# Kernel tuning notes

Measured on AMD Instinct MI355X. Metric: run time of the kernel, lower is better.

Reference implementation:

```python
import jax, jax.numpy as jnp
import numpy as np

# Domain bounds and training nu-range (from init_kwargs)
X_MIN, X_MAX = -1.0, 1.0
Y_MIN, Y_MAX = -1.0, 1.0
T_MIN, T_MAX = 0.0, 1.0
NU_MIN, NU_MAX = 0.01, 0.1

LAYERS = [4, 256, 256, 256, 256, 2]
N = 16384  # collocation points


def setup_inputs() -> dict:
    key = jax.random.key(0)
    ks = jax.random.split(key, 4 + 2 * (len(LAYERS) - 1))
    inp = {
        'x': jax.random.uniform(ks[0], (N, 1), minval=X_MIN, maxval=X_MAX, dtype=jnp.float32),
        'y': jax.random.uniform(ks[1], (N, 1), minval=Y_MIN, maxval=Y_MAX, dtype=jnp.float32),
        't': jax.random.uniform(ks[2], (N, 1), minval=T_MIN, maxval=T_MAX, dtype=jnp.float32),
        'nu': jax.random.uniform(ks[3], (N, 1), minval=NU_MIN, maxval=NU_MAX, dtype=jnp.float32),
    }
    # glorot_normal weights, zero biases (keras Dense defaults)
    for i in range(len(LAYERS) - 1):
        fan_in, fan_out = LAYERS[i], LAYERS[i + 1]
        std = (2.0 / (fan_in + fan_out)) ** 0.5
        inp[f'W{i}'] = std * jax.random.normal(ks[4 + 2 * i], (fan_in, fan_out), dtype=jnp.float32)
        inp[f'b{i}'] = jnp.zeros((fan_out,), dtype=jnp.float32)
    return inp


def _net(pt, nu, params):
    """MLP forward for a single point. pt: (3,) = (x, y, t); nu: scalar. Returns (2,) = (u, v)."""
    x, y, t = pt[0], pt[1], pt[2]
    h = jnp.stack([
        2.0 * (x - X_MIN) / (X_MAX - X_MIN) - 1.0,
        2.0 * (y - Y_MIN) / (Y_MAX - Y_MIN) - 1.0,
        2.0 * (t - T_MIN) / (T_MAX - T_MIN) - 1.0,
        2.0 * (nu - NU_MIN) / (NU_MAX - NU_MIN) - 1.0,
    ])
    for W, b in params[:-1]:
        z = h @ W + b
        h = z * jax.nn.sigmoid(z)  # swish
    W, b = params[-1]
    return h @ W + b


def _residual_point(pt, nu, params):
    """Burgers PDE residual (f_u, f_v) at one collocation point via nested forward-mode AD."""
    f = lambda p: _net(p, nu, params)
    uv = f(pt)                          # (2,)
    J = jax.jacfwd(f)(pt)               # (2,3): d(u,v)/d(x,y,t)
    H = jax.jacfwd(jax.jacfwd(f))(pt)   # (2,3,3)
    u, v = uv[0], uv[1]
    u_x, u_y, u_t = J[0, 0], J[0, 1], J[0, 2]
    v_x, v_y, v_t = J[1, 0], J[1, 1], J[1, 2]
    u_xx, u_yy = H[0, 0, 0], H[0, 1, 1]
    v_xx, v_yy = H[1, 0, 0], H[1, 1, 1]
    f_u = u_t + u * u_x + v * u_y - nu * (u_xx + u_yy)
    f_v = v_t + u * v_x + v * v_y - nu * (v_xx + v_yy)
    return jnp.stack([f_u, f_v])


def reference(x, y, t, nu, W0, b0, W1, b1, W2, b2, W3, b3, W4, b4):
    params = [(W0, b0), (W1, b1), (W2, b2), (W3, b3), (W4, b4)]
    pts = jnp.concatenate([x, y, t], axis=1)  # (N, 3)
    res = jax.vmap(lambda p, n: _residual_point(p, n, params))(pts, nu[:, 0])
    return res  # (N, 2) = [f_u, f_v]
```

## Files before the change

### kernel.cpp

```cpp
#include <hip/hip_runtime.h>

typedef _Float16 f16;
typedef _Float16 v8hf __attribute__((ext_vector_type(8)));
typedef _Float16 v4hf __attribute__((ext_vector_type(4)));
typedef _Float16 v2hf __attribute__((ext_vector_type(2)));
typedef __fp16   v2pk __attribute__((ext_vector_type(2)));
typedef float    v4f  __attribute__((ext_vector_type(4)));

#define NPTS 16384
#define PTS  16
#define NLAYER_ELEMS 65536

__device__ __forceinline__ v2hf pkrtz(float a, float b) {
    v2pk r = __builtin_amdgcn_cvt_pkrtz(a, b);
    return __builtin_bit_cast(v2hf, r);
}

__device__ __forceinline__ int swz(int m, int j) {
    return m * 256 + ((((j >> 3) ^ (m & 7)) << 3) | (j & 7));
}

__global__ void pack_weights(const float* __restrict__ W1, const float* __restrict__ W2,
                             const float* __restrict__ W3, f16* __restrict__ bh,
                             f16* __restrict__ bl) {
    const int b  = blockIdx.x;
    const int kg = b & 3;
    const int q  = (b >> 2) & 3;
    const int ks = (b >> 4) & 7;
    const int L  = b >> 7;
    const float* W = (L == 0) ? W1 : (L == 1) ? W2 : W3;
    const int n   = q * 64 + (threadIdx.x & 63);
    const int kk0 = kg * 8 + (threadIdx.x >> 6) * 2;
    f16 h[2], l[2];
    #pragma unroll
    for (int i = 0; i < 2; ++i) {
        float w = W[(ks * 32 + kk0 + i) * 256 + n];
        f16 hh = (f16)w;
        h[i] = hh;
        l[i] = (f16)(w - (float)hh);
    }
    size_t off = (size_t)L * NLAYER_ELEMS + (size_t)(ks * 256 + n) * 32 + kk0;
    *(v2hf*)(bh + off) = *(v2hf*)h;
    *(v2hf*)(bl + off) = *(v2hf*)l;
}

__device__ __forceinline__ void store_split(const float* a, int m, int nb,
                                            f16* __restrict__ Ah, f16* __restrict__ Al) {
    v2hf h01 = pkrtz(a[0], a[1]);
    v2hf h23 = pkrtz(a[2], a[3]);
    v2hf l01 = pkrtz(a[0] - (float)h01[0], a[1] - (float)h01[1]);
    v2hf l23 = pkrtz(a[2] - (float)h23[0], a[3] - (float)h23[1]);
    v4hf hi = { h01[0], h01[1], h23[0], h23[1] };
    v4hf lo = { l01[0], l01[1], l23[0], l23[1] };
    int idx = swz(m, nb);
    *(v4hf*)&Ah[idx] = hi;
    *(v4hf*)&Al[idx] = lo;
}

__global__ __launch_bounds__(512, 2) void pinn_burgers_kernel(
    const float* __restrict__ gx, const float* __restrict__ gy,
    const float* __restrict__ gt, const float* __restrict__ gnu,
    const float* __restrict__ W0, const float* __restrict__ b0,
    const float* __restrict__ b1, const float* __restrict__ b2,
    const float* __restrict__ b3,
    const float* __restrict__ W4, const float* __restrict__ b4,
    const f16* __restrict__ bh, const f16* __restrict__ bl,
    float* __restrict__ out)
{
    extern __shared__ f16 smem[];
    f16* __restrict__ Ah = smem;
    f16* __restrict__ Al = smem + 96 * 256;
    float* red = (float*)(smem + 2 * 96 * 256);
    float* pin = red + PTS * 12;

    const int tid  = threadIdx.x;
    const int lane = tid & 63;
    const int wv   = tid >> 6;
    const int ln   = lane & 15;
    const int quad = lane >> 4;
    const int lnx  = ln & 7;
    const int p0   = blockIdx.x * PTS;

    if (tid < 4 * PTS) {
        int c = tid >> 4, p = tid & 15;
        const float* src = (c == 0) ? gx : (c == 1) ? gy : (c == 2) ? gt : gnu;
        pin[c * PTS + p] = src[p0 + p];
    }
    __syncthreads();

    {
        const int j0 = wv * 32 + ln * 2;
        const int ph = quad * 4;
        float w00[2], w01[2], w02[2], w03[2], bb[2];
        #pragma unroll
        for (int e = 0; e < 2; ++e) {
            int j = j0 + e;
            w00[e] = W0[j]; w01[e] = W0[256 + j]; w02[e] = W0[512 + j]; w03[e] = W0[768 + j];
            bb[e] = b0[j];
        }
        #pragma unroll
        for (int pp = 0; pp < 4; ++pp) {
            int p = ph + pp;
            float hx = pin[0 * PTS + p];
            float hy = pin[1 * PTS + p];
            float ht = 2.f * pin[2 * PTS + p] - 1.f;
            float hn = 2.f * (pin[3 * PTS + p] - 0.01f) * (1.f / 0.09f) - 1.f;
            float a[6][2];
            #pragma unroll
            for (int e = 0; e < 2; ++e) {
                float z  = hx * w00[e] + hy * w01[e] + ht * w02[e] + hn * w03[e] + bb[e];
                float zx = w00[e], zy = w01[e], zt = 2.f * w02[e];
                float s  = 1.f / (1.f + __expf(-z));
                float g1 = s + z * s * (1.f - s);
                float g2 = s * (1.f - s) * (2.f + z * (1.f - 2.f * s));
                a[0][e] = z * s;
                a[1][e] = g1 * zx; a[2][e] = g1 * zy; a[3][e] = g1 * zt;
                a[4][e] = g2 * zx * zx; a[5][e] = g2 * zy * zy;
            }
            #pragma unroll
            for (int c = 0; c < 6; ++c) {
                int idx = swz(c * PTS + p, j0);
                v2hf hh = pkrtz(a[c][0], a[c][1]);
                v2hf ll = pkrtz(a[c][0] - (float)hh[0], a[c][1] - (float)hh[1]);
                *(v2hf*)&Ah[idx] = hh;
                *(v2hf*)&Al[idx] = ll;
            }
        }
    }
    __syncthreads();

    const float* bias_ptr[3] = { b1, b2, b3 };
    for (int L = 0; L < 3; ++L) {
        const f16* __restrict__ bhL = bh + (size_t)L * NLAYER_ELEMS;
        const f16* __restrict__ blL = bl + (size_t)L * NLAYER_ELEMS;
        const float* __restrict__ bv = bias_ptr[L];

        v4f acc[2][6];
        #pragma unroll
        for (int t = 0; t < 2; ++t)
            #pragma unroll
            for (int mt = 0; mt < 6; ++mt)
                acc[t][mt] = (v4f){0.f, 0.f, 0.f, 0.f};

        #pragma unroll 2
        for (int ks = 0; ks < 8; ++ks) {
            const int cb = (((4 * ks + quad) ^ lnx) << 3);
            v8hf a_h[6], a_l[6];
            #pragma unroll
            for (int mt = 0; mt < 6; ++mt) {
                const int rb = (mt * 16 + ln) * 256 + cb;
                a_h[mt] = *(const v8hf*)&Ah[rb];
                a_l[mt] = *(const v8hf*)&Al[rb];
            }
            v8hf w_h[2], w_l[2];
            #pragma unroll
            for (int t = 0; t < 2; ++t) {
                int n = wv * 32 + t * 16 + ln;
                size_t o = (size_t)(ks * 256 + n) * 32 + quad * 8;
                w_h[t] = *(const v8hf*)(bhL + o);
                w_l[t] = *(const v8hf*)(blL + o);
            }
            #pragma unroll
            for (int t = 0; t < 2; ++t)
                #pragma unroll
                for (int mt = 0; mt < 6; ++mt) {
                    acc[t][mt] = __builtin_amdgcn_mfma_f32_16x16x32_f16(w_h[t], a_h[mt], acc[t][mt], 0, 0, 0);
                    acc[t][mt] = __builtin_amdgcn_mfma_f32_16x16x32_f16(w_h[t], a_l[mt], acc[t][mt], 0, 0, 0);
                    acc[t][mt] = __builtin_amdgcn_mfma_f32_16x16x32_f16(w_l[t], a_h[mt], acc[t][mt], 0, 0, 0);
                }
        }
        __syncthreads();

        #pragma unroll
        for (int t = 0; t < 2; ++t) {
            const int nb = wv * 32 + t * 16 + quad * 4;
            const float4 bq = *(const float4*)(bv + nb);
            const float bb[4] = { bq.x, bq.y, bq.z, bq.w };
            float av[6][4];
            #pragma unroll
            for (int r = 0; r < 4; ++r) {
                float z   = acc[t][0][r] + bb[r];
                float zx  = acc[t][1][r];
                float zy  = acc[t][2][r];
                float zt  = acc[t][3][r];
                float zxx = acc[t][4][r];
                float zyy = acc[t][5][r];
                float s  = 1.f / (1.f + __expf(-z));
                float g1 = s + z * s * (1.f - s);
                float g2 = s * (1.f - s) * (2.f + z * (1.f - 2.f * s));
                av[0][r] = z * s;
                av[1][r] = g1 * zx;
                av[2][r] = g1 * zy;
                av[3][r] = g1 * zt;
                av[4][r] = g2 * zx * zx + g1 * zxx;
                av[5][r] = g2 * zy * zy + g1 * zyy;
            }
            #pragma unroll
            for (int c = 0; c < 6; ++c)
                store_split(av[c], c * 16 + ln, nb, Ah, Al);
        }
        __syncthreads();
    }

    #pragma unroll
    for (int d = 0; d < 24; ++d) {
        int D  = wv * 24 + d;
        int p  = D / 12;
        int rm = D % 12;
        int c  = rm >> 1;
        int o  = rm & 1;
        int m  = c * 16 + p;
        int k0 = lane * 4;
        int idx = swz(m, k0);
        v4hf hh = *(v4hf*)&Ah[idx];
        v4hf ll = *(v4hf*)&Al[idx];
        float partial = 0.f;
        #pragma unroll
        for (int i = 0; i < 4; ++i)
            partial += ((float)hh[i] + (float)ll[i]) * W4[(k0 + i) * 2 + o];
        #pragma unroll
        for (int off = 32; off > 0; off >>= 1)
            partial += __shfl_down(partial, off);
        if (lane == 0)
            red[p * 12 + rm] = partial + ((c == 0) ? b4[o] : 0.f);
    }
    __syncthreads();

    if (tid < PTS) {
        int p = tid;
        float u   = red[p*12+0],  v   = red[p*12+1];
        float ux  = red[p*12+2],  vx  = red[p*12+3];
        float uy  = red[p*12+4],  vy  = red[p*12+5];
        float ut  = red[p*12+6],  vt  = red[p*12+7];
        float uxx = red[p*12+8],  vxx = red[p*12+9];
        float uyy = red[p*12+10], vyy = red[p*12+11];
        float nuv = pin[3 * PTS + p];
        float fu = ut + u * ux + v * uy - nuv * (uxx + uyy);
        float fv = vt + u * vx + v * vy - nuv * (vxx + vyy);
        out[(p0 + p) * 2 + 0] = fu;
        out[(p0 + p) * 2 + 1] = fv;
    }
}

extern "C" void kernel_launch(void* const* d_in, const int* in_sizes, int n_in,
                              void* d_out, int out_size, void* d_ws, size_t ws_size,
                              hipStream_t stream) {
    const float* x  = (const float*)d_in[0];
    const float* y  = (const float*)d_in[1];
    const float* t  = (const float*)d_in[2];
    const float* nu = (const float*)d_in[3];
    const float* W0 = (const float*)d_in[4];
    const float* b0 = (const float*)d_in[5];
    const float* W1 = (const float*)d_in[6];
    const float* b1 = (const float*)d_in[7];
    const float* W2 = (const float*)d_in[8];
    const float* b2 = (const float*)d_in[9];
    const float* W3 = (const float*)d_in[10];
    const float* b3 = (const float*)d_in[11];
    const float* W4 = (const float*)d_in[12];
    const float* b4 = (const float*)d_in[13];
    float* o = (float*)d_out;

    f16* bh = (f16*)d_ws;
    f16* bl = bh + 3 * (size_t)NLAYER_ELEMS;

    const size_t shmem = 2 * 96 * 256 * sizeof(f16) + (PTS * 12 + 4 * PTS) * sizeof(float);
    static bool attr_set = false;
    (void)hipFuncSetAttribute((const void*)pinn_burgers_kernel,
                              hipFuncAttributeMaxDynamicSharedMemorySize, (int)shmem);

    hipLaunchKernelGGL(pack_weights, dim3(384), dim3(256), 0, stream, W1, W2, W3, bh, bl);
    hipLaunchKernelGGL(pinn_burgers_kernel, dim3(NPTS / PTS), dim3(512), shmem, stream,
                       x, y, t, nu, W0, b0, b1, b2, b3, W4, b4, bh, bl, o);
}
```

Baseline: 224.3 us.

## Retile hidden-layer MFMA work as 2x4 wave grid with interleaved row layout

Reorganizes the eight waves into a 2 (points) by 4 (neurons) grid so each wave computes 64 output neurons over 48 rows instead of 32 neurons over 96 rows. Activation rows are reordered so each 16-row tile mixes channels of 8 points, and the epilogue uses lane shuffles to reunite value and derivative channels for the same point. The aim is fewer LDS activation reads per MFMA, in exchange for more global weight fragments per wave, extra shuffles and lane selects in the epilogue.

```diff
diff --git a/kernel.cpp b/kernel.cpp
--- a/kernel.cpp
+++ b/kernel.cpp
@@ -18,6 +18,10 @@
 
 __device__ __forceinline__ int swz(int m, int j) {
     return m * 256 + ((((j >> 3) ^ (m & 7)) << 3) | (j & 7));
+}
+
+__device__ __forceinline__ int rowmap(int c, int p) {
+    return (p >> 3) * 48 + c * 8 + (p & 7);
 }
 
 __global__ void pack_weights(const float* __restrict__ W1, const float* __restrict__ W2,
@@ -76,6 +80,8 @@
     const int tid  = threadIdx.x;
     const int lane = tid & 63;
     const int wv   = tid >> 6;
+    const int nw   = wv & 3;
+    const int mw   = wv >> 2;
     const int ln   = lane & 15;
     const int quad = lane >> 4;
     const int lnx  = ln & 7;
@@ -89,8 +95,8 @@
     __syncthreads();
 
     {
-        const int j0 = wv * 32 + ln * 2;
-        const int ph = quad * 4;
+        const int j0 = nw * 64 + (lane & 31) * 2;
+        const int ph = mw * 8 + (lane >> 5) * 4;
         float w00[2], w01[2], w02[2], w03[2], bb[2];
         #pragma unroll
         for (int e = 0; e < 2; ++e) {
@@ -119,7 +125,7 @@
             }
             #pragma unroll
             for (int c = 0; c < 6; ++c) {
-                int idx = swz(c * PTS + p, j0);
+                int idx = swz(rowmap(c, p), j0);
                 v2hf hh = pkrtz(a[c][0], a[c][1]);
                 v2hf ll = pkrtz(a[c][0] - (float)hh[0], a[c][1] - (float)hh[1]);
                 *(v2hf*)&Ah[idx] = hh;
@@ -129,41 +135,42 @@
     }
     __syncthreads();
 
+    const int rbase = mw * 48;
     const float* bias_ptr[3] = { b1, b2, b3 };
     for (int L = 0; L < 3; ++L) {
         const f16* __restrict__ bhL = bh + (size_t)L * NLAYER_ELEMS;
         const f16* __restrict__ blL = bl + (size_t)L * NLAYER_ELEMS;
         const float* __restrict__ bv = bias_ptr[L];
 
-        v4f acc[2][6];
-        #pragma unroll
-        for (int t = 0; t < 2; ++t)
-            #pragma unroll
-            for (int mt = 0; mt < 6; ++mt)
+        v4f acc[4][3];
+        #pragma unroll
+        for (int t = 0; t < 4; ++t)
+            #pragma unroll
+            for (int mt = 0; mt < 3; ++mt)
                 acc[t][mt] = (v4f){0.f, 0.f, 0.f, 0.f};
 
         #pragma unroll 2
         for (int ks = 0; ks < 8; ++ks) {
             const int cb = (((4 * ks + quad) ^ lnx) << 3);
-            v8hf a_h[6], a_l[6];
-            #pragma unroll
-            for (int mt = 0; mt < 6; ++mt) {
-                const int rb = (mt * 16 + ln) * 256 + cb;
+            v8hf a_h[3], a_l[3];
+            #pragma unroll
+            for (int mt = 0; mt < 3; ++mt) {
+                const int rb = (rbase + mt * 16 + ln) * 256 + cb;
                 a_h[mt] = *(const v8hf*)&Ah[rb];
                 a_l[mt] = *(const v8hf*)&Al[rb];
             }
-            v8hf w_h[2], w_l[2];
-            #pragma unroll
-            for (int t = 0; t < 2; ++t) {
-                int n = wv * 32 + t * 16 + ln;
+            v8hf w_h[4], w_l[4];
+            #pragma unroll
+            for (int t = 0; t < 4; ++t) {
+                int n = nw * 64 + t * 16 + ln;
                 size_t o = (size_t)(ks * 256 + n) * 32 + quad * 8;
                 w_h[t] = *(const v8hf*)(bhL + o);
                 w_l[t] = *(const v8hf*)(blL + o);
             }
             #pragma unroll
-            for (int t = 0; t < 2; ++t)
+            for (int t = 0; t < 4; ++t)
                 #pragma unroll
-                for (int mt = 0; mt < 6; ++mt) {
+                for (int mt = 0; mt < 3; ++mt) {
                     acc[t][mt] = __builtin_amdgcn_mfma_f32_16x16x32_f16(w_h[t], a_h[mt], acc[t][mt], 0, 0, 0);
                     acc[t][mt] = __builtin_amdgcn_mfma_f32_16x16x32_f16(w_h[t], a_l[mt], acc[t][mt], 0, 0, 0);
                     acc[t][mt] = __builtin_amdgcn_mfma_f32_16x16x32_f16(w_l[t], a_h[mt], acc[t][mt], 0, 0, 0);
@@ -171,33 +178,33 @@
         }
         __syncthreads();
 
-        #pragma unroll
-        for (int t = 0; t < 2; ++t) {
-            const int nb = wv * 32 + t * 16 + quad * 4;
+        const bool isA = (ln < 8);
+        #pragma unroll
+        for (int t = 0; t < 4; ++t) {
+            const int nb = nw * 64 + t * 16 + quad * 4;
             const float4 bq = *(const float4*)(bv + nb);
-            const float bb[4] = { bq.x, bq.y, bq.z, bq.w };
-            float av[6][4];
+            const float bsel[4] = { isA ? bq.x : 0.f, isA ? bq.y : 0.f,
+                                    isA ? bq.z : 0.f, isA ? bq.w : 0.f };
+            float a0v[4], a1v[4], a2v[4];
             #pragma unroll
             for (int r = 0; r < 4; ++r) {
-                float z   = acc[t][0][r] + bb[r];
-                float zx  = acc[t][1][r];
-                float zy  = acc[t][2][r];
-                float zt  = acc[t][3][r];
-                float zxx = acc[t][4][r];
-                float zyy = acc[t][5][r];
+                float accv0 = acc[t][0][r] + bsel[r];
+                float acc1  = acc[t][1][r];
+                float acc2  = acc[t][2][r];
+                float o0 = __shfl_xor(accv0, 8);
+                float o1 = __shfl_xor(acc1, 8);
+                float z  = isA ? accv0 : o0;
+                float sq = isA ? o0    : o1;
                 float s  = 1.f / (1.f + __expf(-z));
                 float g1 = s + z * s * (1.f - s);
                 float g2 = s * (1.f - s) * (2.f + z * (1.f - 2.f * s));
-                av[0][r] = z * s;
-                av[1][r] = g1 * zx;
-                av[2][r] = g1 * zy;
-                av[3][r] = g1 * zt;
-                av[4][r] = g2 * zx * zx + g1 * zxx;
-                av[5][r] = g2 * zy * zy + g1 * zyy;
-            }
-            #pragma unroll
-            for (int c = 0; c < 6; ++c)
-                store_split(av[c], c * 16 + ln, nb, Ah, Al);
+                a0v[r] = isA ? (z * s) : (g1 * accv0);
+                a1v[r] = g1 * acc1;
+                a2v[r] = g2 * sq * sq + g1 * acc2;
+            }
+            store_split(a0v, rbase + ln,      nb, Ah, Al);
+            store_split(a1v, rbase + 16 + ln, nb, Ah, Al);
+            store_split(a2v, rbase + 32 + ln, nb, Ah, Al);
         }
         __syncthreads();
     }
@@ -209,7 +216,7 @@
         int rm = D % 12;
         int c  = rm >> 1;
         int o  = rm & 1;
-        int m  = c * 16 + p;
+        int m  = rowmap(c, p);
         int k0 = lane * 4;
         int idx = swz(m, k0);
         v4hf hh = *(v4hf*)&Ah[idx];
@@ -265,7 +272,6 @@
     f16* bl = bh + 3 * (size_t)NLAYER_ELEMS;
 
     const size_t shmem = 2 * 96 * 256 * sizeof(f16) + (PTS * 12 + 4 * PTS) * sizeof(float);
-    static bool attr_set = false;
     (void)hipFuncSetAttribute((const void*)pinn_burgers_kernel,
                               hipFuncAttributeMaxDynamicSharedMemorySize, (int)shmem);
 
```

Result: slower. 271.9 us (+21.2%).
